# Kernel optimization log

Hardware: AMD Instinct MI355X
Metric: run time of the kernel (lower is better)

Reference implementation:

```python
import jax, jax.numpy as jnp
import numpy as np

NPOINT = 2048  # S after transition-down (init npoint)
NSAMPLE = 16   # K neighbors (init nsample)
EPS = 1e-5     # BatchNorm eps


def _conv1d(w, b, x):  # w [O,I], x [B,I,N] -> [B,O,N]
    y = jnp.einsum('oi,bin->bon', w, x)
    return y if b is None else y + b[None, :, None]


def _conv2d(w, b, x):  # w [O,I], x [B,I,S,K] -> [B,O,S,K]
    y = jnp.einsum('oi,bisk->bosk', w, x)
    return y if b is None else y + b[None, :, None, None]


def _gather(x, idx):  # x [B,C,N], idx [B,S] -> [B,C,S]
    return jax.vmap(lambda xb, ib: xb[:, ib])(x, idx)


def _group(x, idx):  # x [B,C,N], idx [B,S,K] -> [B,C,S,K]
    return jax.vmap(lambda xb, ib: xb[:, ib])(x, idx)


def _fps(xyz_bnc, S):  # farthest point sampling, start at index 0 (deterministic)
    B, N, _ = xyz_bnc.shape
    def body(carry, _):
        dist, far = carry
        centroid = jnp.take_along_axis(xyz_bnc, far[:, None, None], axis=1)  # [B,1,3]
        d = jnp.sum((xyz_bnc - centroid) ** 2, axis=-1)  # [B,N]
        dist = jnp.minimum(dist, d)
        nxt = jnp.argmax(dist, axis=-1).astype(jnp.int32)
        return (dist, nxt), far
    init = (jnp.full((B, N), 1e10, xyz_bnc.dtype), jnp.zeros((B,), jnp.int32))
    _, idxs = jax.lax.scan(body, init, None, length=S)
    return jnp.transpose(idxs)  # [B,S]


def _knn(k, query, pts):  # query [B,S,3], pts [B,N,3] -> idx [B,S,k]
    d2 = (jnp.sum(query ** 2, -1)[..., None] + jnp.sum(pts ** 2, -1)[:, None, :]
          - 2.0 * jnp.einsum('bsc,bnc->bsn', query, pts))
    _, idx = jax.lax.top_k(-d2, k)
    return idx


def _bn(x, gamma, beta):  # training-mode batchnorm over (B, spatial) per channel
    axes = (0,) + tuple(range(2, x.ndim))
    m = jnp.mean(x, axes, keepdims=True)
    v = jnp.var(x, axes, keepdims=True)
    shp = (1, -1) + (1,) * (x.ndim - 2)
    return gamma.reshape(shp) * (x - m) / jnp.sqrt(v + EPS) + beta.reshape(shp)


def _forward(xyz, points, td_w, td_b, td_gamma, td_beta,
             blk_before_w, blk_before_b, blk_qkv_w,
             blk_pos_w1, blk_pos_b1, blk_pos_w2, blk_pos_b2,
             blk_attn_w1, blk_attn_b1, blk_attn_w2, blk_attn_b2,
             blk_after_w, blk_after_b):
    S, K = NPOINT, NSAMPLE
    xyz_t = jnp.transpose(xyz, (0, 2, 1))  # [B,N,3]
    # ---- PointTransformerTransitionDown ----
    fps_idx = _fps(xyz_t, S)                       # [B,S]
    new_xyz = _gather(xyz, fps_idx)                # [B,3,S]
    new_xyz_t = jnp.transpose(new_xyz, (0, 2, 1))  # [B,S,3]
    gidx = _knn(K, new_xyz_t, xyz_t)               # [B,S,K]
    grouped_xyz = _group(xyz, gidx) - new_xyz[:, :, :, None]   # [B,3,S,K]
    grouped = jnp.concatenate([_group(points, gidx), grouped_xyz], axis=1)  # [B,D+3,S,K]
    h = jax.nn.relu(_bn(_conv2d(td_w, td_b, grouped), td_gamma, td_beta))
    pts = jnp.max(h, axis=-1)  # [B,out,S]
    # ---- PointTransformerResBlocks ----
    sgidx = _knn(K, new_xyz_t, new_xyz_t)          # self-KNN [B,S,K]
    gxyz = new_xyz[:, :, :, None] - _group(new_xyz, sgidx)  # [B,3,S,K]
    num_attn = blk_before_w.shape[0]
    for i in range(num_attn):
        rel = _conv2d(blk_pos_w2[i], blk_pos_b2[i],
                      jax.nn.relu(_conv2d(blk_pos_w1[i], blk_pos_b1[i], gxyz)))  # [B,mid,S,K]
        p = _conv1d(blk_before_w[i], blk_before_b[i], pts)   # [B,mid,S]
        qkv = _conv1d(blk_qkv_w[i], None, p)                 # [B,3*mid,S]
        q, k_, v = jnp.split(qkv, 3, axis=1)
        qk_rel = q[:, :, :, None] - _group(k_, sgidx)        # [B,mid,S,K]
        v = _group(v, sgidx) + rel
        sim = _conv2d(blk_attn_w2[i], blk_attn_b2[i],
                      jax.nn.relu(_conv2d(blk_attn_w1[i], blk_attn_b1[i], qk_rel + rel)))
        attn = jax.nn.softmax(sim, axis=-1)                  # softmax over neighbors
        agg = jnp.sum(attn * v, axis=-1)                     # [B,mid,S]
        pts = pts + _conv1d(blk_after_w[i], blk_after_b[i], agg)
    return new_xyz, pts


def setup_inputs() -> dict:
    key = jax.random.key(0)
    ks = jax.random.split(key, 20)
    B, N, Din, Dout, mid, A = 4, 8192, 64, 128, 32, 2
    r = lambda k, s, sc: sc * jax.random.normal(k, s, dtype=jnp.float32)
    return {
        'xyz': r(ks[0], (B, 3, N), 1.0),
        'points': r(ks[1], (B, Din, N), 1.0),
        'td_w': r(ks[2], (Dout, Din + 3), 0.1), 'td_b': r(ks[3], (Dout,), 0.02),
        'td_gamma': jnp.ones((Dout,), jnp.float32), 'td_beta': jnp.zeros((Dout,), jnp.float32),
        'blk_before_w': r(ks[4], (A, mid, Dout), 0.1), 'blk_before_b': r(ks[5], (A, mid), 0.02),
        'blk_qkv_w': r(ks[6], (A, 3 * mid, mid), 0.1),
        'blk_pos_w1': r(ks[7], (A, 64, 3), 0.1), 'blk_pos_b1': r(ks[8], (A, 64), 0.02),
        'blk_pos_w2': r(ks[9], (A, mid, 64), 0.1), 'blk_pos_b2': r(ks[10], (A, mid), 0.02),
        'blk_attn_w1': r(ks[11], (A, 4 * mid, mid), 0.1), 'blk_attn_b1': r(ks[12], (A, 4 * mid), 0.02),
        'blk_attn_w2': r(ks[13], (A, mid, 4 * mid), 0.1), 'blk_attn_b2': r(ks[14], (A, mid), 0.02),
        'blk_after_w': r(ks[15], (A, Dout, mid), 0.1), 'blk_after_b': r(ks[16], (A, Dout), 0.02),
    }


def reference(xyz, points, td_w, td_b, td_gamma, td_beta,
              blk_before_w, blk_before_b, blk_qkv_w,
              blk_pos_w1, blk_pos_b1, blk_pos_w2, blk_pos_b2,
              blk_attn_w1, blk_attn_b1, blk_attn_w2, blk_attn_b2,
              blk_after_w, blk_after_b):
    return _forward(xyz, points, td_w, td_b, td_gamma, td_beta,
                    blk_before_w, blk_before_b, blk_qkv_w,
                    blk_pos_w1, blk_pos_b1, blk_pos_w2, blk_pos_b2,
                    blk_attn_w1, blk_attn_b1, blk_attn_w2, blk_attn_b2,
                    blk_after_w, blk_after_b)
```

## Files before the change

kernel.cpp:

```cpp
#include <hip/hip_runtime.h>

#define BB 4
#define NN 8192
#define SS 2048
#define KK 16

typedef float v2f __attribute__((ext_vector_type(2)));

__device__ __forceinline__ float wred_max(float v) {
  float s;
  s = __int_as_float(__builtin_amdgcn_update_dpp(0, __float_as_int(v), 0x111, 0xf, 0xf, true)); v = fmaxf(v, s);
  s = __int_as_float(__builtin_amdgcn_update_dpp(0, __float_as_int(v), 0x112, 0xf, 0xf, true)); v = fmaxf(v, s);
  s = __int_as_float(__builtin_amdgcn_update_dpp(0, __float_as_int(v), 0x114, 0xf, 0xf, true)); v = fmaxf(v, s);
  s = __int_as_float(__builtin_amdgcn_update_dpp(0, __float_as_int(v), 0x118, 0xf, 0xf, true)); v = fmaxf(v, s);
  s = __int_as_float(__builtin_amdgcn_update_dpp(0, __float_as_int(v), 0x142, 0xf, 0xf, true)); v = fmaxf(v, s);
  s = __int_as_float(__builtin_amdgcn_update_dpp(0, __float_as_int(v), 0x143, 0xf, 0xf, true)); v = fmaxf(v, s);
  return v;
}
__device__ __forceinline__ float wred_min(float v) {
  float s;
  s = __int_as_float(__builtin_amdgcn_update_dpp(0, __float_as_int(v), 0x111, 0xf, 0xf, true)); v = fminf(v, s);
  s = __int_as_float(__builtin_amdgcn_update_dpp(0, __float_as_int(v), 0x112, 0xf, 0xf, true)); v = fminf(v, s);
  s = __int_as_float(__builtin_amdgcn_update_dpp(0, __float_as_int(v), 0x114, 0xf, 0xf, true)); v = fminf(v, s);
  s = __int_as_float(__builtin_amdgcn_update_dpp(0, __float_as_int(v), 0x118, 0xf, 0xf, true)); v = fminf(v, s);
  s = __int_as_float(__builtin_amdgcn_update_dpp(0, __float_as_int(v), 0x142, 0xf, 0xf, true)); v = fminf(v, s);
  s = __int_as_float(__builtin_amdgcn_update_dpp(0, __float_as_int(v), 0x143, 0xf, 0xf, true)); v = fminf(v, s);
  return v;
}
__device__ __forceinline__ int morton8(float x, float y, float z,
                                       float mnx, float mny, float mnz,
                                       float scx, float scy, float scz) {
  int qx = min(7, (int)((x - mnx) * scx));
  int qy = min(7, (int)((y - mny) * scy));
  int qz = min(7, (int)((z - mnz) * scz));
  return (qx&1) | ((qy&1)<<1) | ((qz&1)<<2)
       | ((qx&2)<<2) | ((qy&2)<<3) | ((qz&2)<<4)
       | ((qx&4)<<4) | ((qy&4)<<5) | ((qz&4)<<6);
}

#define FTH 512
#define FPT (NN/FTH)
#define TRB 256
#define SPB 124
__global__ __launch_bounds__(FTH, 1) void fps_kernel(
    const float* __restrict__ xyz,
    const float* __restrict__ points,
    const float* __restrict__ td_w,
    const float* __restrict__ bw,
    const float* __restrict__ qw,
    const float* __restrict__ aw1,
    const float* __restrict__ fw,
    float* __restrict__ out_newxyz,
    float* __restrict__ ptst,
    float4* __restrict__ csorted,
    float*  __restrict__ caabb,
    float4* __restrict__ qsorted,
    float*  __restrict__ qaabb,
    float* __restrict__ td_wT,
    float* __restrict__ bwT,
    float* __restrict__ qwT,
    float* __restrict__ aw1T,
    float* __restrict__ fwT,
    int* __restrict__ spin_flag)
{
  #pragma clang fp contract(off)
  const int blk = blockIdx.x;
  const int tid = threadIdx.x;
  const int wave = tid >> 6;
  const int lane = tid & 63;
  __shared__ __align__(16) float4 sxyz[NN];
  __shared__ __align__(16) unsigned long long skey[2][8];
  __shared__ int smi[SS];
  __shared__ float sred[8*6];
  __shared__ float tile[32][33];

  if (blk >= BB) {
    if (blk < BB + TRB) {
      if (blk == BB && tid == 0) spin_flag[8] = 0;
      const int x = tid & 31, yy = tid >> 5;
      for (int q = 0; q < 8; ++q) {
        const int tj = (blk - BB)*8 + q;
        const int tn = tj & 255, tc = (tj >> 8) & 1, tb = tj >> 9;
        const int n0 = tn*32, c0 = tc*32;
        __syncthreads();
        tile[yy][x]    = points[(tb*64 + c0+yy)*NN + n0+x];
        tile[yy+16][x] = points[(tb*64 + c0+yy+16)*NN + n0+x];
        __syncthreads();
        ptst[(tb*NN + n0+yy)*64 + c0+x]    = tile[x][yy];
        ptst[(tb*NN + n0+yy+16)*64 + c0+x] = tile[x][yy+16];
      }
      if (blk == BB + 8) {
        for (int idx = tid; idx < 128*67; idx += FTH) {
          int c = idx / 67, i = idx - c*67;
          td_wT[i*128 + c] = td_w[idx];
        }
        for (int l = 0; l < 2; ++l) {
          for (int idx = tid; idx < 32*128; idx += FTH) {
            int r = idx >> 7, c = idx & 127;
            bwT[l*4096 + c*32 + r] = bw[l*4096 + idx];
          }
          for (int idx = tid; idx < 96*32; idx += FTH) {
            int r = idx >> 5, c = idx & 31;
            qwT[l*3072 + c*96 + r] = qw[l*3072 + idx];
          }
          for (int idx = tid; idx < 128*32; idx += FTH) {
            int r = idx >> 5, c = idx & 31;
            aw1T[l*4096 + c*128 + r] = aw1[l*4096 + idx];
            fwT [l*4096 + c*128 + r] = fw [l*4096 + idx];
          }
        }
      }
      if (blk - BB < BB) {
        const int b2 = blk - BB;
        const float* xb2 = xyz + b2*3*NN;
        float tx[FPT], ty[FPT], tz[FPT];
        #pragma unroll
        for (int j = 0; j < FPT; ++j) {
          int i = tid + j*FTH;
          tx[j] = xb2[i]; ty[j] = xb2[NN+i]; tz[j] = xb2[2*NN+i];
        }
        float mnx = tx[0], mxx = tx[0], mny = ty[0], mxy = ty[0], mnz = tz[0], mxz = tz[0];
        #pragma unroll
        for (int j = 1; j < FPT; ++j) {
          mnx = fminf(mnx, tx[j]); mxx = fmaxf(mxx, tx[j]);
          mny = fminf(mny, ty[j]); mxy = fmaxf(mxy, ty[j]);
          mnz = fminf(mnz, tz[j]); mxz = fmaxf(mxz, tz[j]);
        }
        mnx = wred_min(mnx); mxx = wred_max(mxx);
        mny = wred_min(mny); mxy = wred_max(mxy);
        mnz = wred_min(mnz); mxz = wred_max(mxz);
        if (lane == 63) {
          sred[wave*6+0] = mnx; sred[wave*6+1] = mxx; sred[wave*6+2] = mny;
          sred[wave*6+3] = mxy; sred[wave*6+4] = mnz; sred[wave*6+5] = mxz;
        }
        smi[tid] = 0;
        __syncthreads();
        #pragma unroll
        for (int w = 0; w < 8; ++w) {
          mnx = fminf(mnx, sred[w*6+0]); mxx = fmaxf(mxx, sred[w*6+1]);
          mny = fminf(mny, sred[w*6+2]); mxy = fmaxf(mxy, sred[w*6+3]);
          mnz = fminf(mnz, sred[w*6+4]); mxz = fmaxf(mxz, sred[w*6+5]);
        }
        const float scx = 8.0f / (mxx - mnx + 1e-12f);
        const float scy = 8.0f / (mxy - mny + 1e-12f);
        const float scz = 8.0f / (mxz - mnz + 1e-12f);
        int cells[FPT];
        #pragma unroll
        for (int j = 0; j < FPT; ++j) {
          cells[j] = morton8(tx[j], ty[j], tz[j], mnx, mny, mnz, scx, scy, scz);
          atomicAdd(&smi[cells[j]], 1);
        }
        __syncthreads();
        for (int d = 1; d < 512; d <<= 1) {
          int v = smi[tid];
          int a = (tid >= d) ? smi[tid - d] : 0;
          __syncthreads();
          smi[tid] = v + a;
          __syncthreads();
        }
        { int excl = (tid == 0) ? 0 : smi[tid - 1]; smi[512 + tid] = excl; }
        __syncthreads();
        #pragma unroll
        for (int j = 0; j < FPT; ++j) {
          int pos = atomicAdd(&smi[512 + cells[j]], 1);
          csorted[b2*NN + pos] = make_float4(tx[j], ty[j], tz[j], __int_as_float(tid + j*FTH));
        }
        __syncthreads();
        for (int sl = wave; sl < 32; sl += 8) {
          float a0x=1e30f, a1x=-1e30f, a0y=1e30f, a1y=-1e30f, a0z=1e30f, a1z=-1e30f;
          #pragma unroll
          for (int t = 0; t < 4; ++t) {
            float4 c = csorted[b2*NN + sl*256 + lane*4 + t];
            a0x = fminf(a0x, c.x); a1x = fmaxf(a1x, c.x);
            a0y = fminf(a0y, c.y); a1y = fmaxf(a1y, c.y);
            a0z = fminf(a0z, c.z); a1z = fmaxf(a1z, c.z);
          }
          a0x = wred_min(a0x); a1x = wred_max(a1x);
          a0y = wred_min(a0y); a1y = wred_max(a1y);
          a0z = wred_min(a0z); a1z = wred_max(a1z);
          if (lane == 63) {
            float* o = caabb + (b2*32 + sl)*8;
            o[0]=a0x; o[1]=a1x; o[2]=a0y; o[3]=a1y; o[4]=a0z; o[5]=a1z;
          }
        }
      }
      return;
    }
    if (tid >= 64) return;
    const int s0 = atomicAdd(spin_flag, 0);
    float a0 = 1.0f + tid, a1 = 2.0f, a2 = 3.0f, a3 = 4.0f;
    for (int outer = 0; outer < 50000; ++outer) {
      #pragma unroll
      for (int u = 0; u < 256; ++u) {
        a0 = fmaf(a0, 1.0000001f, 1e-7f);
        a1 = fmaf(a1, 0.9999999f, 2e-7f);
        a2 = fmaf(a2, 1.0000002f, 3e-7f);
        a3 = fmaf(a3, 0.9999998f, 4e-7f);
      }
      if (atomicAdd(spin_flag, 0) - s0 >= BB) break;
    }
    asm volatile("" :: "v"(a0), "v"(a1), "v"(a2), "v"(a3));
    return;
  }

  const int b = blk;
  const float* xb = xyz + b*3*NN;

  float tx[FPT], ty[FPT], tz[FPT];
  #pragma unroll
  for (int j = 0; j < FPT; ++j) {
    int i = tid + j*FTH;
    tx[j] = xb[i]; ty[j] = xb[NN+i]; tz[j] = xb[2*NN+i];
  }
  float mnx = tx[0], mxx = tx[0], mny = ty[0], mxy = ty[0], mnz = tz[0], mxz = tz[0];
  #pragma unroll
  for (int j = 1; j < FPT; ++j) {
    mnx = fminf(mnx, tx[j]); mxx = fmaxf(mxx, tx[j]);
    mny = fminf(mny, ty[j]); mxy = fmaxf(mxy, ty[j]);
    mnz = fminf(mnz, tz[j]); mxz = fmaxf(mxz, tz[j]);
  }
  mnx = wred_min(mnx); mxx = wred_max(mxx);
  mny = wred_min(mny); mxy = wred_max(mxy);
  mnz = wred_min(mnz); mxz = wred_max(mxz);
  if (lane == 63) {
    sred[wave*6+0] = mnx; sred[wave*6+1] = mxx; sred[wave*6+2] = mny;
    sred[wave*6+3] = mxy; sred[wave*6+4] = mnz; sred[wave*6+5] = mxz;
  }
  smi[tid] = 0;
  __syncthreads();
  #pragma unroll
  for (int w = 0; w < 8; ++w) {
    mnx = fminf(mnx, sred[w*6+0]); mxx = fmaxf(mxx, sred[w*6+1]);
    mny = fminf(mny, sred[w*6+2]); mxy = fmaxf(mxy, sred[w*6+3]);
    mnz = fminf(mnz, sred[w*6+4]); mxz = fmaxf(mxz, sred[w*6+5]);
  }
  const float scx = 8.0f / (mxx - mnx + 1e-12f);
  const float scy = 8.0f / (mxy - mny + 1e-12f);
  const float scz = 8.0f / (mxz - mnz + 1e-12f);
  int cells[FPT];
  #pragma unroll
  for (int j = 0; j < FPT; ++j) {
    cells[j] = morton8(tx[j], ty[j], tz[j], mnx, mny, mnz, scx, scy, scz);
    atomicAdd(&smi[cells[j]], 1);
  }
  __syncthreads();
  for (int d = 1; d < 512; d <<= 1) {
    int v = smi[tid];
    int a = (tid >= d) ? smi[tid - d] : 0;
    __syncthreads();
    smi[tid] = v + a;
    __syncthreads();
  }
  {
    int excl = (tid == 0) ? 0 : smi[tid - 1];
    smi[512 + tid] = excl;
  }
  __syncthreads();
  #pragma unroll
  for (int j = 0; j < FPT; ++j) {
    int pos = atomicAdd(&smi[512 + cells[j]], 1);
    sxyz[pos] = make_float4(tx[j], ty[j], tz[j], 0.0f);
  }
  __syncthreads();
  v2f px[FPT/2], py[FPT/2], pz[FPT/2], dist[FPT/2];
  float bx0, bx1, by0, by1, bz0, bz1;
  {
    float4 c0 = sxyz[tid*FPT];
    bx0 = bx1 = c0.x; by0 = by1 = c0.y; bz0 = bz1 = c0.z;
    #pragma unroll
    for (int e = 0; e < FPT; ++e) {
      float4 cc = sxyz[tid*FPT + e];
      ((float*)px)[e] = cc.x; ((float*)py)[e] = cc.y; ((float*)pz)[e] = cc.z;
      ((float*)dist)[e] = 1e10f;
      bx0 = fminf(bx0, cc.x); bx1 = fmaxf(bx1, cc.x);
      by0 = fminf(by0, cc.y); by1 = fmaxf(by1, cc.y);
      bz0 = fminf(bz0, cc.z); bz1 = fmaxf(bz1, cc.z);
    }
  }
  float dmax = 1e10f;
  int   beste = 0;
  float cx = xb[0], cy = xb[NN], cz = xb[2*NN];
  __syncthreads();
  for (int it = 1; it < SS; ++it) {
    const int buf = it & 1;
    float gx = fmaxf(fmaxf(bx0 - cx, cx - bx1), 0.0f);
    float gy = fmaxf(fmaxf(by0 - cy, cy - by1), 0.0f);
    float gz = fmaxf(fmaxf(bz0 - cz, cz - bz1), 0.0f);
    float lb = gx*gx + gy*gy; lb = lb + gz*gz;
    if (lb * 0.99999f < dmax) {
      v2f cx2 = {cx, cx}, cy2 = {cy, cy}, cz2 = {cz, cz};
      v2f vmax = {-1.0f, -1.0f};
      #pragma unroll
      for (int j = 0; j < FPT/2; ++j) {
        v2f dx = px[j] - cx2, dy = py[j] - cy2, dz = pz[j] - cz2;
        v2f d = dx*dx + dy*dy;
        d = d + dz*dz;
        v2f nd = __builtin_elementwise_min(dist[j], d);
        dist[j] = nd;
        vmax = __builtin_elementwise_max(vmax, nd);
      }
      float mloc = fmaxf(vmax.x, vmax.y);
      int ce[FPT/2];
      #pragma unroll
      for (int j = 0; j < FPT/2; ++j) {
        int c = 0x7FFFFFFF;
        if (dist[j].y == mloc) c = 2*j + 1;
        if (dist[j].x == mloc) c = 2*j;
        ce[j] = c;
      }
      #pragma unroll
      for (int st = FPT/4; st >= 1; st >>= 1) {
        #pragma unroll
        for (int j = 0; j < st; ++j) ce[j] = ce[j] < ce[j+st] ? ce[j] : ce[j+st];
      }
      dmax = mloc;
      beste = ce[0];
    }
    float wm = dmax;
    wm = wred_max(wm);
    wm = __int_as_float(__builtin_amdgcn_readlane(__float_as_int(wm), 63));
    unsigned long long em = __ballot(dmax == wm);
    int lw = (int)__ffsll((unsigned long long)em) - 1;
    int bi_w = __builtin_amdgcn_readlane((tid << 4) + beste, lw);
    if (lane == 63) skey[buf][wave] = ((unsigned long long)__float_as_uint(wm) << 32) | (unsigned)~bi_w;
    __syncthreads();
    const ulonglong2* kp = (const ulonglong2*)&skey[buf][0];
    ulonglong2 k01 = kp[0], k23 = kp[1], k45 = kp[2], k67 = kp[3];
    unsigned long long m0 = k01.x > k01.y ? k01.x : k01.y;
    unsigned long long m1 = k23.x > k23.y ? k23.x : k23.y;
    unsigned long long m2 = k45.x > k45.y ? k45.x : k45.y;
    unsigned long long m3 = k67.x > k67.y ? k67.x : k67.y;
    unsigned long long ma = m0 > m1 ? m0 : m1;
    unsigned long long mb = m2 > m3 ? m2 : m3;
    unsigned long long mk = ma > mb ? ma : mb;
    int mi = (int)(~(unsigned)mk);
    float4 c = sxyz[mi];
    if (tid == 0) smi[it] = mi;
    cx = c.x; cy = c.y; cz = c.z;
  }
  __syncthreads();
  for (int it = tid; it < SS; it += FTH) {
    float x, y, z;
    if (it == 0) { x = xb[0]; y = xb[NN]; z = xb[2*NN]; }
    else { float4 c = sxyz[smi[it]]; x = c.x; y = c.y; z = c.z; }
    out_newxyz[(b*3+0)*SS + it] = x;
    out_newxyz[(b*3+1)*SS + it] = y;
    out_newxyz[(b*3+2)*SS + it] = z;
  }
  float4 qp4[4]; int qj4[4], qc4[4];
  #pragma unroll
  for (int k2 = 0; k2 < 4; ++k2) {
    int j = tid + k2*FTH;
    float4 p;
    if (j == 0) p = make_float4(xb[0], xb[NN], xb[2*NN], 0.0f);
    else        p = sxyz[smi[j]];
    qp4[k2] = p; qj4[k2] = j;
  }
  __syncthreads();
  smi[tid] = 0;
  __syncthreads();
  #pragma unroll
  for (int k2 = 0; k2 < 4; ++k2) {
    qc4[k2] = morton8(qp4[k2].x, qp4[k2].y, qp4[k2].z, mnx, mny, mnz, scx, scy, scz);
    atomicAdd(&smi[qc4[k2]], 1);
  }
  __syncthreads();
  for (int d = 1; d < 512; d <<= 1) {
    int v = smi[tid];
    int a = (tid >= d) ? smi[tid - d] : 0;
    __syncthreads();
    smi[tid] = v + a;
    __syncthreads();
  }
  { int excl = (tid == 0) ? 0 : smi[tid - 1]; smi[512 + tid] = excl; }
  __syncthreads();
  #pragma unroll
  for (int k2 = 0; k2 < 4; ++k2) {
    int pos = atomicAdd(&smi[512 + qc4[k2]], 1);
    qsorted[b*SS + pos] = make_float4(qp4[k2].x, qp4[k2].y, qp4[k2].z, __int_as_float(qj4[k2]));
  }
  __syncthreads();
  {
    float a0x=1e30f, a1x=-1e30f, a0y=1e30f, a1y=-1e30f, a0z=1e30f, a1z=-1e30f;
    #pragma unroll
    for (int t = 0; t < 4; ++t) {
      float4 c = qsorted[b*SS + wave*256 + lane*4 + t];
      a0x = fminf(a0x, c.x); a1x = fmaxf(a1x, c.x);
      a0y = fminf(a0y, c.y); a1y = fmaxf(a1y, c.y);
      a0z = fminf(a0z, c.z); a1z = fmaxf(a1z, c.z);
    }
    a0x = wred_min(a0x); a1x = wred_max(a1x);
    a0y = wred_min(a0y); a1y = wred_max(a1y);
    a0z = wred_min(a0z); a1z = wred_max(a1z);
    if (lane == 63) {
      float* o = qaabb + (b*8 + wave)*8;
      o[0]=a0x; o[1]=a1x; o[2]=a0y; o[3]=a1y; o[4]=a0z; o[5]=a1z;
    }
  }
  if (tid == 0) atomicAdd(spin_flag, 1);
}

#define KTH 512
__global__ __launch_bounds__(KTH) void knn_kernel(
    const float4* __restrict__ qsorted,
    const float*  __restrict__ qaabb,
    const float4* __restrict__ csorted,
    const float*  __restrict__ caabb,
    int* __restrict__ out1,
    int* __restrict__ out2)
{
  #pragma clang fp contract(off)
  __shared__ float4 sc[8][256];
  __shared__ int    sidx[8][256];
  __shared__ float  smd[8*64*17];
  __shared__ int    smj[8*64*17];
  const int bid = blockIdx.x;
  const int half = bid >> 7;
  const int rem = bid & 127;
  const int b = rem >> 5;
  const int wslot = rem & 31;
  const int wave = threadIdx.x >> 6, lane = threadIdx.x & 63;
  const float4* cand = half ? (qsorted + b*SS) : (csorted + b*NN);
  const float*  aabb = half ? (qaabb + b*8*8) : (caabb + b*32*8);
  const int nsl = half ? 8 : 32;
  const int sh = half ? (wslot >> 2) : wslot;
  const int nj = nsl >> 3;
  int* outidx = half ? out2 : out1;

  float4 q = qsorted[b*SS + wslot*64 + lane];
  const int orig_s = __float_as_int(q.w);
  const float qx = q.x, qy = q.y, qz = q.z;
  float sq = qx*qx + qy*qy; sq = sq + qz*qz;
  float d16[16]; int i16[16];
  #pragma unroll
  for (int j = 0; j < 16; ++j) { d16[j] = 1e30f; i16[j] = 0x7FFFFFFF; }

  for (int jj = 0; jj < nj; ++jj) {
    const int j = wave + jj*8;
    const int off = (j + 1) >> 1;
    const int s = (sh + ((j & 1) ? off : -off)) & (nsl - 1);
    const float* ab = aabb + s*8;
    float gx = fmaxf(fmaxf(ab[0] - qx, qx - ab[1]), 0.0f);
    float gy = fmaxf(fmaxf(ab[2] - qy, qy - ab[3]), 0.0f);
    float gz = fmaxf(fmaxf(ab[4] - qz, qz - ab[5]), 0.0f);
    float lbnd = gx*gx + gy*gy; lbnd = lbnd + gz*gz;
    bool skip = (lbnd * 0.9999f - 1e-3f) > d16[15];
    if (__all(skip)) continue;
    #pragma unroll
    for (int t = 0; t < 4; ++t) {
      float4 c = cand[s*256 + t*64 + lane];
      float pp = c.x*c.x + c.y*c.y; pp = pp + c.z*c.z;
      sidx[wave][t*64 + lane] = __float_as_int(c.w);
      sc[wave][t*64 + lane] = make_float4(c.x, c.y, c.z, pp);
    }
    for (int t = 0; t < 256; ++t) {
      float4 c = sc[wave][t];
      float qp = qx*c.x + qy*c.y; qp = qp + qz*c.z;
      float d2 = (sq + c.w) - 2.0f*qp;
      if (d2 < d16[15]) {
        d16[15] = d2; i16[15] = sidx[wave][t];
        #pragma unroll
        for (int u = 15; u > 0; --u) {
          if (d16[u] < d16[u-1]) {
            float td = d16[u]; d16[u] = d16[u-1]; d16[u-1] = td;
            int   ti = i16[u]; i16[u] = i16[u-1]; i16[u-1] = ti;
          }
        }
      }
    }
  }
  const int offm = (wave*64 + lane)*17;
  #pragma unroll
  for (int j = 0; j < 16; ++j) { smd[offm+j] = d16[j]; smj[offm+j] = i16[j]; }
  __syncthreads();
  if (wave == 0) {
    int p[8] = {0,0,0,0,0,0,0,0};
    for (int o = 0; o < 16; ++o) {
      float bd = 3e38f; int bi = 0x7FFFFFFF, bw = 0;
      #pragma unroll
      for (int w = 0; w < 8; ++w) {
        float d = smd[(w*64+lane)*17 + p[w]];
        int   i = smj[(w*64+lane)*17 + p[w]];
        if (d < bd || (d == bd && i < bi)) { bd = d; bi = i; bw = w; }
      }
      p[bw]++;
      outidx[(b*SS + orig_s)*KK + o] = bi;
    }
  }
}

__global__ __launch_bounds__(128) void td_kernel(
    const float* __restrict__ ptst,
    const float* __restrict__ xyz,
    const float* __restrict__ newxyz,
    const int* __restrict__ gidx,
    const float* __restrict__ td_wT,
    const float* __restrict__ td_b,
    float* __restrict__ ymax,
    float* __restrict__ psum,
    float* __restrict__ psq)
{
  const int bs = blockIdx.x;
  const int b = bs >> 11, s = bs & (SS-1);
  const int t = threadIdx.x;
  __shared__ int gi[KK];
  __shared__ float g[67*17];
  if (t < KK) gi[t] = gidx[bs*KK + t];
  __syncthreads();
  #pragma unroll
  for (int base = 0; base < 1024; base += 128) {
    int idx = base + t;
    int i = idx & 63, k = idx >> 6;
    g[i*17 + k] = ptst[(b*NN + gi[k])*64 + i];
  }
  if (t < 48) {
    int c = t >> 4, k = t & 15;
    g[(64+c)*17 + k] = xyz[(b*3+c)*NN + gi[k]] - newxyz[(b*3+c)*SS + s];
  }
  __syncthreads();
  float acc[KK];
  #pragma unroll
  for (int k = 0; k < KK; ++k) acc[k] = 0.0f;
  for (int i = 0; i < 67; ++i) {
    float w = td_wT[i*128 + t];
    #pragma unroll
    for (int k = 0; k < KK; ++k) acc[k] = fmaf(w, g[i*17 + k], acc[k]);
  }
  float bias = td_b[t];
  float mx = -1e30f, s1 = 0.f, s2 = 0.f;
  #pragma unroll
  for (int k = 0; k < KK; ++k) {
    float y = acc[k] + bias;
    mx = fmaxf(mx, y);
    s1 += y;
    s2 = fmaf(y, y, s2);
  }
  ymax[bs*128 + t] = mx;
  psum[bs*128 + t] = s1;
  psq [bs*128 + t] = s2;
}

__global__ __launch_bounds__(256) void bn_partial(
    const float* __restrict__ psum, const float* __restrict__ psq,
    float* __restrict__ part1, float* __restrict__ part2,
    const float* __restrict__ gamma, const float* __restrict__ beta,
    float* __restrict__ scale, float* __restrict__ bias,
    int* __restrict__ counter)
{
  const int blk = blockIdx.x, t = threadIdx.x;
  const int c = t & 127, half = t >> 7;
  const float* ps = psum + (blk*64 + half*32)*128;
  const float* pq = psq  + (blk*64 + half*32)*128;
  float s1 = 0.f, s2 = 0.f;
  for (int r = 0; r < 32; ++r) { s1 += ps[r*128 + c]; s2 += pq[r*128 + c]; }
  __shared__ float sh1[256], sh2[256];
  __shared__ int s_last;
  sh1[t] = s1; sh2[t] = s2;
  __syncthreads();
  if (t < 128) {
    part1[blk*128 + t] = sh1[t] + sh1[t+128];
    part2[blk*128 + t] = sh2[t] + sh2[t+128];
  }
  __syncthreads();
  __threadfence();
  if (t == 0) s_last = (atomicAdd(counter, 1) == 127) ? 1 : 0;
  __syncthreads();
  if (!s_last) return;
  __threadfence();
  float f1 = 0.f, f2 = 0.f;
  for (int j = half*64; j < half*64 + 64; ++j) {
    f1 += part1[j*128 + c];
    f2 += part2[j*128 + c];
  }
  sh1[t] = f1; sh2[t] = f2;
  __syncthreads();
  if (t < 128) {
    float a1 = sh1[t] + sh1[t+128];
    float a2 = sh2[t] + sh2[t+128];
    const float n = (float)(BB*SS*KK);
    float mean = a1/n;
    float var  = a2/n - mean*mean;
    float sc = gamma[t] / sqrtf(var + 1e-5f);
    scale[t] = sc;
    bias[t]  = beta[t] - mean*sc;
  }
}

__global__ __launch_bounds__(128) void r1_first(
    const float* __restrict__ ymax,
    const float* __restrict__ scale, const float* __restrict__ bias,
    const float* __restrict__ bwT, const float* __restrict__ bb,
    const float* __restrict__ qwT,
    float* __restrict__ pts,
    float* __restrict__ qkv)
{
  const int bs = blockIdx.x;
  const int t = threadIdx.x;
  __shared__ float pcol[128];
  __shared__ float p[32];
  float v = fmaxf(fmaf(ymax[bs*128 + t], scale[t], bias[t]), 0.0f);
  pts[bs*128 + t] = v;
  pcol[t] = v;
  __syncthreads();
  if (t < 32) {
    float acc = 0.f;
    for (int j = 0; j < 128; ++j) acc = fmaf(bwT[j*32 + t], pcol[j], acc);
    p[t] = acc + bb[t];
  }
  __syncthreads();
  if (t < 96) {
    float acc = 0.f;
    #pragma unroll
    for (int j = 0; j < 32; ++j) acc = fmaf(qwT[j*96 + t], p[j], acc);
    qkv[bs*96 + t] = acc;
  }
}

__global__ __launch_bounds__(128) void r1_kernel(
    const float* __restrict__ pts,
    const float* __restrict__ bwT, const float* __restrict__ bb,
    const float* __restrict__ qwT,
    float* __restrict__ qkv)
{
  const int bs = blockIdx.x;
  const int t = threadIdx.x;
  __shared__ float pcol[128];
  __shared__ float p[32];
  pcol[t] = pts[bs*128 + t];
  __syncthreads();
  if (t < 32) {
    float acc = 0.f;
    for (int j = 0; j < 128; ++j) acc = fmaf(bwT[j*32 + t], pcol[j], acc);
    p[t] = acc + bb[t];
  }
  __syncthreads();
  if (t < 96) {
    float acc = 0.f;
    #pragma unroll
    for (int j = 0; j < 32; ++j) acc = fmaf(qwT[j*96 + t], p[j], acc);
    qkv[bs*96 + t] = acc;
  }
}

__global__ __launch_bounds__(128) void r2_kernel(
    const float* __restrict__ qkv,
    const float* __restrict__ newxyz,
    const int* __restrict__ sgidx,
    const float* __restrict__ pw1, const float* __restrict__ pb1,
    const float* __restrict__ pw2, const float* __restrict__ pb2,
    const float* __restrict__ aw1T, const float* __restrict__ ab1,
    const float* __restrict__ aw2, const float* __restrict__ ab2,
    const float* __restrict__ fwT,  const float* __restrict__ fb,
    float* __restrict__ pts,
    float* __restrict__ outT)
{
  const int bs = blockIdx.x;
  const int b = bs >> 11, s = bs & (SS-1);
  const int t = threadIdx.x;
  __shared__ int sgi[KK];
  __shared__ float qv[32];
  __shared__ float kn[32*17], vn[32*17];
  __shared__ float gx[3*KK];
  __shared__ float h1[64*KK];
  __shared__ float x2[32*KK];
  __shared__ float a1[128*17];
  __shared__ float simb[32*KK];
  __shared__ float agg[32];
  if (t < KK) sgi[t] = sgidx[bs*KK + t];
  __syncthreads();
  if (t < 32) qv[t] = qkv[bs*96 + t];
  for (int idx = t; idx < 32*KK; idx += 128) {
    int k = idx >> 5, c = idx & 31;
    int base = (b*SS + sgi[k])*96;
    kn[c*17+k] = qkv[base + 32 + c];
    vn[c*17+k] = qkv[base + 64 + c];
  }
  if (t < 3*KK) {
    int c = t >> 4, k = t & 15;
    gx[t] = newxyz[(b*3+c)*SS + s] - newxyz[(b*3+c)*SS + sgi[k]];
  }
  __syncthreads();
  for (int idx = t; idx < 64*KK; idx += 128) {
    int c = idx >> 4, k = idx & 15;
    float acc = 0.f;
    #pragma unroll
    for (int j = 0; j < 3; ++j) acc = fmaf(pw1[c*3+j], gx[j*KK+k], acc);
    h1[idx] = fmaxf(acc + pb1[c], 0.0f);
  }
  __syncthreads();
  for (int idx = t; idx < 32*KK; idx += 128) {
    int c = idx >> 4, k = idx & 15;
    float acc = 0.f;
    const float* w = pw2 + c*64;
    for (int j = 0; j < 64; ++j) acc = fmaf(w[j], h1[j*KK+k], acc);
    float r = acc + pb2[c];
    x2[idx] = (qv[c] - kn[c*17+k]) + r;
    vn[c*17+k] = vn[c*17+k] + r;
  }
  __syncthreads();
  {
    float acc[KK];
    #pragma unroll
    for (int k = 0; k < KK; ++k) acc[k] = 0.f;
    for (int j = 0; j < 32; ++j) {
      float wv = aw1T[j*128 + t];
      #pragma unroll
      for (int k = 0; k < KK; ++k) acc[k] = fmaf(wv, x2[j*KK+k], acc[k]);
    }
    float bv = ab1[t];
    #pragma unroll
    for (int k = 0; k < KK; ++k) a1[t*17+k] = fmaxf(acc[k] + bv, 0.0f);
  }
  __syncthreads();
  for (int idx = t; idx < 32*KK; idx += 128) {
    int c = idx >> 4, k = idx & 15;
    float acc = 0.f;
    const float* w = aw2 + c*128;
    for (int j = 0; j < 128; ++j) acc = fmaf(w[j], a1[j*17+k], acc);
    simb[idx] = acc + ab2[c];
  }
  __syncthreads();
  if (t < 32) {
    float m = -1e30f;
    #pragma unroll
    for (int k = 0; k < KK; ++k) m = fmaxf(m, simb[t*KK+k]);
    float sum = 0.f;
    float e[KK];
    #pragma unroll
    for (int k = 0; k < KK; ++k) { e[k] = __expf(simb[t*KK+k] - m); sum += e[k]; }
    float inv = 1.0f / sum;
    float a = 0.f;
    #pragma unroll
    for (int k = 0; k < KK; ++k) a = fmaf(e[k]*inv, vn[t*17+k], a);
    agg[t] = a;
  }
  __syncthreads();
  {
    float acc = 0.f;
    #pragma unroll
    for (int j = 0; j < 32; ++j) acc = fmaf(fwT[j*128 + t], agg[j], acc);
    float val = pts[bs*128 + t] + (acc + fb[t]);
    if (outT) outT[(b*128 + t)*SS + s] = val;
    else      pts[bs*128 + t] = val;
  }
}

extern "C" void kernel_launch(void* const* d_in, const int* in_sizes, int n_in,
                              void* d_out, int out_size, void* d_ws, size_t ws_size,
                              hipStream_t stream) {
  const float* xyz      = (const float*)d_in[0];
  const float* points   = (const float*)d_in[1];
  const float* td_w     = (const float*)d_in[2];
  const float* td_b     = (const float*)d_in[3];
  const float* td_gamma = (const float*)d_in[4];
  const float* td_beta  = (const float*)d_in[5];
  const float* bw  = (const float*)d_in[6];
  const float* bb  = (const float*)d_in[7];
  const float* qw  = (const float*)d_in[8];
  const float* pw1 = (const float*)d_in[9];
  const float* pb1 = (const float*)d_in[10];
  const float* pw2 = (const float*)d_in[11];
  const float* pb2 = (const float*)d_in[12];
  const float* aw1 = (const float*)d_in[13];
  const float* ab1 = (const float*)d_in[14];
  const float* aw2 = (const float*)d_in[15];
  const float* ab2 = (const float*)d_in[16];
  const float* fw  = (const float*)d_in[17];
  const float* fb  = (const float*)d_in[18];
  float* out = (float*)d_out;
  float* out_newxyz = out;
  float* out_pts    = out + BB*3*SS;

  char* w = (char*)d_ws;
  int*   gidx   = (int*)w;   w += BB*SS*KK*sizeof(int);
  int*   sgidx  = (int*)w;   w += BB*SS*KK*sizeof(int);
  float* ymax   = (float*)w; w += BB*128*SS*sizeof(float);
  float* psum   = (float*)w; w += 128*BB*SS*sizeof(float);
  float* psq    = (float*)w; w += 128*BB*SS*sizeof(float);
  float* part1  = (float*)w; w += 128*128*sizeof(float);
  float* part2  = (float*)w; w += 128*128*sizeof(float);
  float* bnscale= (float*)w; w += 256*sizeof(float);
  float* bnbias = (float*)w; w += 256*sizeof(float);
  float* pts    = (float*)w; w += BB*128*SS*sizeof(float);
  float* qkv    = (float*)w; w += BB*96*SS*sizeof(float);
  float* ptst   = (float*)w; w += BB*NN*64*sizeof(float);
  int*   flags  = (int*)w;   w += 256;
  float4* csorted = (float4*)w; w += BB*NN*sizeof(float4);
  float*  caabb   = (float*)w;  w += BB*32*8*sizeof(float);
  float4* qsorted = (float4*)w; w += BB*SS*sizeof(float4);
  float*  qaabb   = (float*)w;  w += BB*8*8*sizeof(float);
  float* td_wT  = (float*)w; w += 67*128*sizeof(float);
  float* bwT    = (float*)w; w += 2*4096*sizeof(float);
  float* qwT    = (float*)w; w += 2*3072*sizeof(float);
  float* aw1T   = (float*)w; w += 2*4096*sizeof(float);
  float* fwT    = (float*)w; w += 2*4096*sizeof(float);

  fps_kernel<<<BB + TRB + SPB, FTH, 0, stream>>>(xyz, points, td_w, bw, qw, aw1, fw,
      out_newxyz, ptst, csorted, caabb, qsorted, qaabb,
      td_wT, bwT, qwT, aw1T, fwT, flags);
  knn_kernel<<<256, KTH, 0, stream>>>(qsorted, qaabb, csorted, caabb, gidx, sgidx);
  td_kernel<<<BB*SS, 128, 0, stream>>>(ptst, xyz, out_newxyz, gidx, td_wT, td_b, ymax, psum, psq);
  bn_partial<<<128, 256, 0, stream>>>(psum, psq, part1, part2,
      td_gamma, td_beta, bnscale, bnbias, &flags[8]);
  r1_first<<<BB*SS, 128, 0, stream>>>(ymax, bnscale, bnbias, bwT, bb, qwT, pts, qkv);
  r2_kernel<<<BB*SS, 128, 0, stream>>>(qkv, out_newxyz, sgidx,
      pw1, pb1, pw2, pb2, aw1T, ab1, aw2, ab2, fwT, fb, pts, nullptr);
  r1_kernel<<<BB*SS, 128, 0, stream>>>(pts, bwT + 4096, bb + 32, qwT + 3072, qkv);
  r2_kernel<<<BB*SS, 128, 0, stream>>>(qkv, out_newxyz, sgidx,
      pw1 + 64*3, pb1 + 64, pw2 + 32*64, pb2 + 32,
      aw1T + 4096, ab1 + 128, aw2 + 32*128, ab2 + 32,
      fwT + 4096, fb + 128, pts, out_pts);
}
```

Before: 2.231 ms.

## Fuse second-block qkv projection into r2 and transpose pw2/aw2 weights

```diff
diff --git a/kernel.cpp b/kernel.cpp
--- a/kernel.cpp
+++ b/kernel.cpp
@@ -50,6 +50,8 @@
     const float* __restrict__ qw,
     const float* __restrict__ aw1,
     const float* __restrict__ fw,
+    const float* __restrict__ aw2,
+    const float* __restrict__ pw2,
     float* __restrict__ out_newxyz,
     float* __restrict__ ptst,
     float4* __restrict__ csorted,
@@ -61,6 +63,8 @@
     float* __restrict__ qwT,
     float* __restrict__ aw1T,
     float* __restrict__ fwT,
+    float* __restrict__ aw2T,
+    float* __restrict__ pw2T,
     int* __restrict__ spin_flag)
 {
   #pragma clang fp contract(off)
@@ -107,6 +111,14 @@
             int r = idx >> 5, c = idx & 31;
             aw1T[l*4096 + c*128 + r] = aw1[l*4096 + idx];
             fwT [l*4096 + c*128 + r] = fw [l*4096 + idx];
+          }
+          for (int idx = tid; idx < 32*128; idx += FTH) {
+            int c = idx >> 7, j = idx & 127;
+            aw2T[l*4096 + j*32 + c] = aw2[l*4096 + idx];
+          }
+          for (int idx = tid; idx < 32*64; idx += FTH) {
+            int c = idx >> 6, j = idx & 63;
+            pw2T[l*2048 + j*32 + c] = pw2[l*2048 + idx];
           }
         }
       }
@@ -616,43 +628,21 @@
   }
 }
 
-__global__ __launch_bounds__(128) void r1_kernel(
-    const float* __restrict__ pts,
-    const float* __restrict__ bwT, const float* __restrict__ bb,
-    const float* __restrict__ qwT,
-    float* __restrict__ qkv)
-{
-  const int bs = blockIdx.x;
-  const int t = threadIdx.x;
-  __shared__ float pcol[128];
-  __shared__ float p[32];
-  pcol[t] = pts[bs*128 + t];
-  __syncthreads();
-  if (t < 32) {
-    float acc = 0.f;
-    for (int j = 0; j < 128; ++j) acc = fmaf(bwT[j*32 + t], pcol[j], acc);
-    p[t] = acc + bb[t];
-  }
-  __syncthreads();
-  if (t < 96) {
-    float acc = 0.f;
-    #pragma unroll
-    for (int j = 0; j < 32; ++j) acc = fmaf(qwT[j*96 + t], p[j], acc);
-    qkv[bs*96 + t] = acc;
-  }
-}
-
 __global__ __launch_bounds__(128) void r2_kernel(
     const float* __restrict__ qkv,
     const float* __restrict__ newxyz,
     const int* __restrict__ sgidx,
     const float* __restrict__ pw1, const float* __restrict__ pb1,
-    const float* __restrict__ pw2, const float* __restrict__ pb2,
+    const float* __restrict__ pw2T, const float* __restrict__ pb2,
     const float* __restrict__ aw1T, const float* __restrict__ ab1,
-    const float* __restrict__ aw2, const float* __restrict__ ab2,
+    const float* __restrict__ aw2T, const float* __restrict__ ab2,
     const float* __restrict__ fwT,  const float* __restrict__ fb,
     float* __restrict__ pts,
-    float* __restrict__ outT)
+    float* __restrict__ outT,
+    const float* __restrict__ nbwT,
+    const float* __restrict__ nbb,
+    const float* __restrict__ nqwT,
+    float* __restrict__ qkv_out)
 {
   const int bs = blockIdx.x;
   const int b = bs >> 11, s = bs & (SS-1);
@@ -666,6 +656,8 @@
   __shared__ float a1[128*17];
   __shared__ float simb[32*KK];
   __shared__ float agg[32];
+  __shared__ float pcol[128];
+  __shared__ float p[32];
   if (t < KK) sgi[t] = sgidx[bs*KK + t];
   __syncthreads();
   if (t < 32) qv[t] = qkv[bs*96 + t];
@@ -691,8 +683,7 @@
   for (int idx = t; idx < 32*KK; idx += 128) {
     int c = idx >> 4, k = idx & 15;
     float acc = 0.f;
-    const float* w = pw2 + c*64;
-    for (int j = 0; j < 64; ++j) acc = fmaf(w[j], h1[j*KK+k], acc);
+    for (int j = 0; j < 64; ++j) acc = fmaf(pw2T[j*32 + c], h1[j*KK+k], acc);
     float r = acc + pb2[c];
     x2[idx] = (qv[c] - kn[c*17+k]) + r;
     vn[c*17+k] = vn[c*17+k] + r;
@@ -715,8 +706,7 @@
   for (int idx = t; idx < 32*KK; idx += 128) {
     int c = idx >> 4, k = idx & 15;
     float acc = 0.f;
-    const float* w = aw2 + c*128;
-    for (int j = 0; j < 128; ++j) acc = fmaf(w[j], a1[j*17+k], acc);
+    for (int j = 0; j < 128; ++j) acc = fmaf(aw2T[j*32 + c], a1[j*17+k], acc);
     simb[idx] = acc + ab2[c];
   }
   __syncthreads();
@@ -735,13 +725,30 @@
     agg[t] = a;
   }
   __syncthreads();
+  float val;
   {
     float acc = 0.f;
     #pragma unroll
     for (int j = 0; j < 32; ++j) acc = fmaf(fwT[j*128 + t], agg[j], acc);
-    float val = pts[bs*128 + t] + (acc + fb[t]);
+    val = pts[bs*128 + t] + (acc + fb[t]);
     if (outT) outT[(b*128 + t)*SS + s] = val;
     else      pts[bs*128 + t] = val;
+  }
+  if (nbwT) {
+    pcol[t] = val;
+    __syncthreads();
+    if (t < 32) {
+      float acc = 0.f;
+      for (int j = 0; j < 128; ++j) acc = fmaf(nbwT[j*32 + t], pcol[j], acc);
+      p[t] = acc + nbb[t];
+    }
+    __syncthreads();
+    if (t < 96) {
+      float acc = 0.f;
+      #pragma unroll
+      for (int j = 0; j < 32; ++j) acc = fmaf(nqwT[j*96 + t], p[j], acc);
+      qkv_out[bs*96 + t] = acc;
+    }
   }
 }
 
@@ -783,6 +790,7 @@
   float* bnbias = (float*)w; w += 256*sizeof(float);
   float* pts    = (float*)w; w += BB*128*SS*sizeof(float);
   float* qkv    = (float*)w; w += BB*96*SS*sizeof(float);
+  float* qkv2   = (float*)w; w += BB*96*SS*sizeof(float);
   float* ptst   = (float*)w; w += BB*NN*64*sizeof(float);
   int*   flags  = (int*)w;   w += 256;
   float4* csorted = (float4*)w; w += BB*NN*sizeof(float4);
@@ -794,20 +802,23 @@
   float* qwT    = (float*)w; w += 2*3072*sizeof(float);
   float* aw1T   = (float*)w; w += 2*4096*sizeof(float);
   float* fwT    = (float*)w; w += 2*4096*sizeof(float);
-
-  fps_kernel<<<BB + TRB + SPB, FTH, 0, stream>>>(xyz, points, td_w, bw, qw, aw1, fw,
+  float* aw2T   = (float*)w; w += 2*4096*sizeof(float);
+  float* pw2T   = (float*)w; w += 2*2048*sizeof(float);
+
+  fps_kernel<<<BB + TRB + SPB, FTH, 0, stream>>>(xyz, points, td_w, bw, qw, aw1, fw, aw2, pw2,
       out_newxyz, ptst, csorted, caabb, qsorted, qaabb,
-      td_wT, bwT, qwT, aw1T, fwT, flags);
+      td_wT, bwT, qwT, aw1T, fwT, aw2T, pw2T, flags);
   knn_kernel<<<256, KTH, 0, stream>>>(qsorted, qaabb, csorted, caabb, gidx, sgidx);
   td_kernel<<<BB*SS, 128, 0, stream>>>(ptst, xyz, out_newxyz, gidx, td_wT, td_b, ymax, psum, psq);
   bn_partial<<<128, 256, 0, stream>>>(psum, psq, part1, part2,
       td_gamma, td_beta, bnscale, bnbias, &flags[8]);
   r1_first<<<BB*SS, 128, 0, stream>>>(ymax, bnscale, bnbias, bwT, bb, qwT, pts, qkv);
   r2_kernel<<<BB*SS, 128, 0, stream>>>(qkv, out_newxyz, sgidx,
-      pw1, pb1, pw2, pb2, aw1T, ab1, aw2, ab2, fwT, fb, pts, nullptr);
-  r1_kernel<<<BB*SS, 128, 0, stream>>>(pts, bwT + 4096, bb + 32, qwT + 3072, qkv);
-  r2_kernel<<<BB*SS, 128, 0, stream>>>(qkv, out_newxyz, sgidx,
-      pw1 + 64*3, pb1 + 64, pw2 + 32*64, pb2 + 32,
-      aw1T + 4096, ab1 + 128, aw2 + 32*128, ab2 + 32,
-      fwT + 4096, fb + 128, pts, out_pts);
-}
+      pw1, pb1, pw2T, pb2, aw1T, ab1, aw2T, ab2, fwT, fb, pts, nullptr,
+      bwT + 4096, bb + 32, qwT + 3072, qkv2);
+  r2_kernel<<<BB*SS, 128, 0, stream>>>(qkv2, out_newxyz, sgidx,
+      pw1 + 64*3, pb1 + 64, pw2T + 2048, pb2 + 32,
+      aw1T + 4096, ab1 + 128, aw2T + 4096, ab2 + 32,
+      fwT + 4096, fb + 128, pts, out_pts,
+      nullptr, nullptr, nullptr, nullptr);
+}
```

Result: slower. 2.368 ms (+6.2%).
